# Kernel tuning notes

Hardware: AMD Instinct MI355X
Metric: run time of the kernel (lower is better)

## Reference

```python
import jax, jax.numpy as jnp
import numpy as np

N_NODES = 50000
N_EDGES = 800000
D = 128


def setup_inputs() -> dict:
    key = jax.random.key(0)
    ks = jax.random.split(key, 7)
    stdv = 1.0 / np.sqrt(D)
    inputs = jax.random.normal(ks[0], (N_NODES, D), dtype=jnp.float32)
    weight = jax.random.uniform(ks[1], (D, D), dtype=jnp.float32, minval=-stdv, maxval=stdv)
    bias = jax.random.uniform(ks[2], (D,), dtype=jnp.float32, minval=-stdv, maxval=stdv)
    alpha = jax.random.uniform(ks[3], (2, 1, 1), dtype=jnp.float32, minval=-3.0, maxval=3.0)
    adj_vals = jax.random.uniform(ks[4], (N_EDGES,), dtype=jnp.float32)
    adj_rows = jax.random.randint(ks[5], (N_EDGES,), 0, N_NODES, dtype=jnp.int32)
    adj_cols = jax.random.randint(ks[6], (N_EDGES,), 0, N_NODES, dtype=jnp.int32)
    return {"inputs": inputs, "weight": weight, "bias": bias, "alpha": alpha,
            "adj_vals": adj_vals, "adj_rows": adj_rows, "adj_cols": adj_cols}


def reference(inputs, weight, bias, alpha, adj_vals, adj_rows, adj_cols):
    n = inputs.shape[0]
    # support = inputs @ weight  (dense GEMM; spmm with dense lhs == matmul)
    support = inputs @ weight                                  # [N, D]
    # output = adj @ support  as COO SpMM: gather source rows, scale, scatter-add
    gathered = support[adj_cols] * adj_vals[:, None]           # [E, D]
    agg = jax.ops.segment_sum(gathered, adj_rows, num_segments=n)  # [N, D]
    # softmax-gated combine of [agg, inputs] (stack order: output first)
    gate = jax.nn.softmax(alpha, axis=0)                       # [2,1,1]
    out = agg * gate[0] + inputs * gate[1]                     # [N, D]
    return jax.nn.elu(out + bias)
```

## Files before the change

kernel.cpp:

```cpp
#include <hip/hip_runtime.h>

#define N_NODES 50000
#define N_EDGES 800000
#define D 128
#define CAP 128

typedef __attribute__((ext_vector_type(8))) short bf16x8;
typedef __attribute__((ext_vector_type(4))) float f32x4;
typedef __attribute__((ext_vector_type(4))) short short4v;

__device__ __forceinline__ short f2bf(float f) {
    unsigned u = __float_as_uint(f);
    unsigned r = u + 0x7FFFu + ((u >> 16) & 1u);
    return (short)(r >> 16);
}
__device__ __forceinline__ float bf2f(short s) {
    return __uint_as_float(((unsigned)(unsigned short)s) << 16);
}

#define SCAT_GROUPS 8
#define SCAT_BPG    392
__global__ __launch_bounds__(256) void gemm_scatter_kernel(
    const float* __restrict__ inp, const float* __restrict__ W,
    short* __restrict__ support,
    const int* __restrict__ rows, const int* __restrict__ cols,
    const float* __restrict__ vals,
    int* __restrict__ cnt, int2* __restrict__ buckets, int nGemmBlocks)
{
    if ((int)blockIdx.x >= nGemmBlocks) {
        const int sbid = (int)blockIdx.x - nGemmBlocks;
        const int g  = sbid & (SCAT_GROUPS - 1);
        const int gi = sbid >> 3;
        const int rowLo = g * (N_NODES / SCAT_GROUPS);
        const int rowHi = rowLo + (N_NODES / SCAT_GROUPS);
        for (int e = gi * 256 + threadIdx.x; e < N_EDGES; e += SCAT_BPG * 256) {
            int r = rows[e];
            if (r >= rowLo && r < rowHi) {
                int p = atomicAdd(&cnt[r], 1);
                if (p < CAP) {
                    int2 pk;
                    pk.x = cols[e];
                    pk.y = __float_as_int(vals[e]);
                    buckets[(size_t)r * CAP + p] = pk;
                }
            }
        }
        return;
    }

    __shared__ short Wt[128][136];
    const int tid = threadIdx.x;

    #pragma unroll
    for (int i = 0; i < 16; ++i) {
        int lin = i * 1024 + tid * 4;
        int k = lin >> 7, c = lin & 127;
        float4 w = *(const float4*)&W[lin];
        Wt[c + 0][k] = f2bf(w.x);
        Wt[c + 1][k] = f2bf(w.y);
        Wt[c + 2][k] = f2bf(w.z);
        Wt[c + 3][k] = f2bf(w.w);
    }
    __syncthreads();

    const int wid = tid >> 6, lane = tid & 63;
    const int lr = lane & 15;
    const int lg = lane >> 4;
    const int m0 = (int)blockIdx.x * 64 + wid * 16;

    int arow = m0 + lr;
    if (arow >= N_NODES) arow = 0;
    const float* aptr = &inp[(size_t)arow * D + lg * 8];

    f32x4 acc[8] = {};
    #pragma unroll
    for (int kc = 0; kc < 4; ++kc) {
        float4 a0 = *(const float4*)(aptr + kc * 32);
        float4 a1 = *(const float4*)(aptr + kc * 32 + 4);
        bf16x8 af;
        af[0] = f2bf(a0.x); af[1] = f2bf(a0.y); af[2] = f2bf(a0.z); af[3] = f2bf(a0.w);
        af[4] = f2bf(a1.x); af[5] = f2bf(a1.y); af[6] = f2bf(a1.z); af[7] = f2bf(a1.w);
        #pragma unroll
        for (int t = 0; t < 8; ++t) {
            const bf16x8 bf = *(const bf16x8*)&Wt[t * 16 + lr][kc * 32 + lg * 8];
            acc[t] = __builtin_amdgcn_mfma_f32_16x16x32_bf16(af, bf, acc[t], 0, 0, 0);
        }
    }
    #pragma unroll
    for (int t = 0; t < 8; ++t) {
        #pragma unroll
        for (int r = 0; r < 4; ++r) {
            int orow = m0 + lg * 4 + r;
            if (orow < N_NODES)
                support[(size_t)orow * D + t * 16 + lr] = f2bf(acc[t][r]);
        }
    }
}

__global__ __launch_bounds__(256) void agg_fused(
    const short* __restrict__ support, const int* __restrict__ cnt,
    const int2* __restrict__ buckets,
    const float* __restrict__ inp, const float* __restrict__ bias,
    const float* __restrict__ alpha, float* __restrict__ out)
{
    const int wv = (blockIdx.x * 256 + threadIdx.x) >> 6;
    const int lane = threadIdx.x & 63;
    if (wv >= N_NODES) return;
    const int half = lane >> 5;
    const int li = lane & 31;

    int n = cnt[wv];
    if (n > CAP) n = CAP;
    const int start = wv * CAP;
    const int end   = start + n;

    const float4 x = *(const float4*)&inp[(size_t)wv * D + li * 4];
    const float4 b4 = *(const float4*)&bias[li * 4];
    const float a0 = alpha[0], a1 = alpha[1];

    float4 acc = make_float4(0.f, 0.f, 0.f, 0.f);
    int e = start;
    for (; e + 8 <= end; e += 8) {
        int2 p0 = buckets[e + 0 + half];
        int2 p1 = buckets[e + 2 + half];
        int2 p2 = buckets[e + 4 + half];
        int2 p3 = buckets[e + 6 + half];
        short4v s0 = *(const short4v*)&support[(size_t)p0.x * D + li * 4];
        short4v s1 = *(const short4v*)&support[(size_t)p1.x * D + li * 4];
        short4v s2 = *(const short4v*)&support[(size_t)p2.x * D + li * 4];
        short4v s3 = *(const short4v*)&support[(size_t)p3.x * D + li * 4];
        float v0 = __int_as_float(p0.y), v1 = __int_as_float(p1.y);
        float v2 = __int_as_float(p2.y), v3 = __int_as_float(p3.y);
        acc.x += v0 * bf2f(s0[0]) + v1 * bf2f(s1[0]) + v2 * bf2f(s2[0]) + v3 * bf2f(s3[0]);
        acc.y += v0 * bf2f(s0[1]) + v1 * bf2f(s1[1]) + v2 * bf2f(s2[1]) + v3 * bf2f(s3[1]);
        acc.z += v0 * bf2f(s0[2]) + v1 * bf2f(s1[2]) + v2 * bf2f(s2[2]) + v3 * bf2f(s3[2]);
        acc.w += v0 * bf2f(s0[3]) + v1 * bf2f(s1[3]) + v2 * bf2f(s2[3]) + v3 * bf2f(s3[3]);
    }
    for (; e < end; e += 2) {
        int idx = e + half;
        int2 p = (idx < end) ? buckets[idx] : make_int2(0, 0);
        float v = __int_as_float(p.y);
        short4v s = *(const short4v*)&support[(size_t)p.x * D + li * 4];
        acc.x += v * bf2f(s[0]);
        acc.y += v * bf2f(s[1]);
        acc.z += v * bf2f(s[2]);
        acc.w += v * bf2f(s[3]);
    }

    acc.x += __shfl_xor(acc.x, 32);
    acc.y += __shfl_xor(acc.y, 32);
    acc.z += __shfl_xor(acc.z, 32);
    acc.w += __shfl_xor(acc.w, 32);

    const float m = fmaxf(a0, a1);
    const float e0 = __expf(a0 - m), e1 = __expf(a1 - m);
    const float inv = 1.f / (e0 + e1);
    const float g0 = e0 * inv, g1 = e1 * inv;

    float t0 = acc.x * g0 + x.x * g1 + b4.x;
    float t1 = acc.y * g0 + x.y * g1 + b4.y;
    float t2 = acc.z * g0 + x.z * g1 + b4.z;
    float t3 = acc.w * g0 + x.w * g1 + b4.w;
    float r0 = t0 > 0.f ? t0 : (__expf(t0) - 1.f);
    float r1 = t1 > 0.f ? t1 : (__expf(t1) - 1.f);
    float r2 = t2 > 0.f ? t2 : (__expf(t2) - 1.f);
    float r3 = t3 > 0.f ? t3 : (__expf(t3) - 1.f);

    float2 o = (half == 0) ? make_float2(r0, r1) : make_float2(r2, r3);
    *(float2*)&out[(size_t)wv * D + li * 4 + half * 2] = o;
}

extern "C" void kernel_launch(void* const* d_in, const int* in_sizes, int n_in,
                              void* d_out, int out_size, void* d_ws, size_t ws_size,
                              hipStream_t stream)
{
    const float* inp   = (const float*)d_in[0];
    const float* W     = (const float*)d_in[1];
    const float* bias  = (const float*)d_in[2];
    const float* alpha = (const float*)d_in[3];
    const float* vals  = (const float*)d_in[4];
    const int*   rows  = (const int*)d_in[5];
    const int*   cols  = (const int*)d_in[6];
    float* out = (float*)d_out;

    short* support = (short*)d_ws;
    int*   cnt     = (int*)(support + (size_t)N_NODES * D);
    int2*  buckets = (int2*)(cnt + N_NODES);

    const int nGemmBlocks = (N_NODES + 63) / 64;
    const int nScatBlocks = SCAT_GROUPS * SCAT_BPG;

    (void)hipMemsetAsync(cnt, 0, (size_t)N_NODES * sizeof(int), stream);

    gemm_scatter_kernel<<<nGemmBlocks + nScatBlocks, 256, 0, stream>>>(
        inp, W, support, rows, cols, vals, cnt, buckets, nGemmBlocks);
    agg_fused<<<(N_NODES * 64 + 255) / 256, 256, 0, stream>>>(
        support, cnt, buckets, inp, bias, alpha, out);
}
```

Measured before the change: 171.1 us.

## Precompute bf16 transposed weight in a prep kernel and flatten edge scatter

```diff
diff --git a/kernel.cpp b/kernel.cpp
--- a/kernel.cpp
+++ b/kernel.cpp
@@ -18,50 +18,78 @@
     return __uint_as_float(((unsigned)(unsigned short)s) << 16);
 }
 
+__global__ __launch_bounds__(256) void prep_zero(const float* __restrict__ W,
+                                                 short* __restrict__ Wt,
+                                                 int* __restrict__ cnt)
+{
+    const int b = blockIdx.x, t = threadIdx.x;
+    if (b < 8) {
+        __shared__ short Ls[128][17];
+        #pragma unroll
+        for (int i = 0; i < 8; ++i) {
+            int lin = i * 256 + t;
+            int kk = lin >> 7;
+            int c  = lin & 127;
+            Ls[c][kk] = f2bf(W[(b * 16 + kk) * 128 + c]);
+        }
+        __syncthreads();
+        #pragma unroll
+        for (int i = 0; i < 8; ++i) {
+            int lin = i * 256 + t;
+            int c  = lin >> 4;
+            int kk = lin & 15;
+            Wt[c * 128 + b * 16 + kk] = Ls[c][kk];
+        }
+    } else {
+        int idx = (b - 8) * 256 + t;
+        if (idx < N_NODES) cnt[idx] = 0;
+    }
+}
+
 #define SCAT_GROUPS 8
-#define SCAT_BPG    392
+#define SCAT_BPG    784
 __global__ __launch_bounds__(256) void gemm_scatter_kernel(
-    const float* __restrict__ inp, const float* __restrict__ W,
+    const float* __restrict__ inp, const short* __restrict__ Wt,
     short* __restrict__ support,
     const int* __restrict__ rows, const int* __restrict__ cols,
     const float* __restrict__ vals,
     int* __restrict__ cnt, int2* __restrict__ buckets, int nGemmBlocks)
 {
+    const int tid = threadIdx.x;
     if ((int)blockIdx.x >= nGemmBlocks) {
         const int sbid = (int)blockIdx.x - nGemmBlocks;
         const int g  = sbid & (SCAT_GROUPS - 1);
         const int gi = sbid >> 3;
         const int rowLo = g * (N_NODES / SCAT_GROUPS);
         const int rowHi = rowLo + (N_NODES / SCAT_GROUPS);
-        for (int e = gi * 256 + threadIdx.x; e < N_EDGES; e += SCAT_BPG * 256) {
-            int r = rows[e];
-            if (r >= rowLo && r < rowHi) {
-                int p = atomicAdd(&cnt[r], 1);
-                if (p < CAP) {
-                    int2 pk;
-                    pk.x = cols[e];
-                    pk.y = __float_as_int(vals[e]);
-                    buckets[(size_t)r * CAP + p] = pk;
-                }
-            }
+        const int base = gi * 1024;
+        int e0 = base + tid, e1 = e0 + 256, e2 = e0 + 512, e3 = e0 + 768;
+        int r0 = (e0 < N_EDGES) ? rows[e0] : -1;
+        int r1 = (e1 < N_EDGES) ? rows[e1] : -1;
+        int r2 = (e2 < N_EDGES) ? rows[e2] : -1;
+        int r3 = (e3 < N_EDGES) ? rows[e3] : -1;
+        if (r0 >= rowLo && r0 < rowHi) {
+            int p = atomicAdd(&cnt[r0], 1);
+            if (p < CAP) buckets[(size_t)r0 * CAP + p] =
+                make_int2(cols[e0], __float_as_int(vals[e0]));
+        }
+        if (r1 >= rowLo && r1 < rowHi) {
+            int p = atomicAdd(&cnt[r1], 1);
+            if (p < CAP) buckets[(size_t)r1 * CAP + p] =
+                make_int2(cols[e1], __float_as_int(vals[e1]));
+        }
+        if (r2 >= rowLo && r2 < rowHi) {
+            int p = atomicAdd(&cnt[r2], 1);
+            if (p < CAP) buckets[(size_t)r2 * CAP + p] =
+                make_int2(cols[e2], __float_as_int(vals[e2]));
+        }
+        if (r3 >= rowLo && r3 < rowHi) {
+            int p = atomicAdd(&cnt[r3], 1);
+            if (p < CAP) buckets[(size_t)r3 * CAP + p] =
+                make_int2(cols[e3], __float_as_int(vals[e3]));
         }
         return;
     }
-
-    __shared__ short Wt[128][136];
-    const int tid = threadIdx.x;
-
-    #pragma unroll
-    for (int i = 0; i < 16; ++i) {
-        int lin = i * 1024 + tid * 4;
-        int k = lin >> 7, c = lin & 127;
-        float4 w = *(const float4*)&W[lin];
-        Wt[c + 0][k] = f2bf(w.x);
-        Wt[c + 1][k] = f2bf(w.y);
-        Wt[c + 2][k] = f2bf(w.z);
-        Wt[c + 3][k] = f2bf(w.w);
-    }
-    __syncthreads();
 
     const int wid = tid >> 6, lane = tid & 63;
     const int lr = lane & 15;
@@ -72,18 +100,28 @@
     if (arow >= N_NODES) arow = 0;
     const float* aptr = &inp[(size_t)arow * D + lg * 8];
 
+    float4 a[8];
+    #pragma unroll
+    for (int kc = 0; kc < 4; ++kc) {
+        a[2 * kc + 0] = *(const float4*)(aptr + kc * 32);
+        a[2 * kc + 1] = *(const float4*)(aptr + kc * 32 + 4);
+    }
+    bf16x8 af[4];
+    #pragma unroll
+    for (int kc = 0; kc < 4; ++kc) {
+        af[kc][0] = f2bf(a[2*kc].x);   af[kc][1] = f2bf(a[2*kc].y);
+        af[kc][2] = f2bf(a[2*kc].z);   af[kc][3] = f2bf(a[2*kc].w);
+        af[kc][4] = f2bf(a[2*kc+1].x); af[kc][5] = f2bf(a[2*kc+1].y);
+        af[kc][6] = f2bf(a[2*kc+1].z); af[kc][7] = f2bf(a[2*kc+1].w);
+    }
+
     f32x4 acc[8] = {};
     #pragma unroll
     for (int kc = 0; kc < 4; ++kc) {
-        float4 a0 = *(const float4*)(aptr + kc * 32);
-        float4 a1 = *(const float4*)(aptr + kc * 32 + 4);
-        bf16x8 af;
-        af[0] = f2bf(a0.x); af[1] = f2bf(a0.y); af[2] = f2bf(a0.z); af[3] = f2bf(a0.w);
-        af[4] = f2bf(a1.x); af[5] = f2bf(a1.y); af[6] = f2bf(a1.z); af[7] = f2bf(a1.w);
         #pragma unroll
         for (int t = 0; t < 8; ++t) {
-            const bf16x8 bf = *(const bf16x8*)&Wt[t * 16 + lr][kc * 32 + lg * 8];
-            acc[t] = __builtin_amdgcn_mfma_f32_16x16x32_bf16(af, bf, acc[t], 0, 0, 0);
+            const bf16x8 bf = *(const bf16x8*)&Wt[(t * 16 + lr) * 128 + kc * 32 + lg * 8];
+            acc[t] = __builtin_amdgcn_mfma_f32_16x16x32_bf16(af[kc], bf, acc[t], 0, 0, 0);
         }
     }
     #pragma unroll
@@ -184,16 +222,16 @@
     float* out = (float*)d_out;
 
     short* support = (short*)d_ws;
-    int*   cnt     = (int*)(support + (size_t)N_NODES * D);
+    short* Wt      = support + (size_t)N_NODES * D;
+    int*   cnt     = (int*)(Wt + 128 * 128);
     int2*  buckets = (int2*)(cnt + N_NODES);
 
     const int nGemmBlocks = (N_NODES + 63) / 64;
     const int nScatBlocks = SCAT_GROUPS * SCAT_BPG;
 
-    (void)hipMemsetAsync(cnt, 0, (size_t)N_NODES * sizeof(int), stream);
-
+    prep_zero<<<8 + (N_NODES + 255) / 256, 256, 0, stream>>>(W, Wt, cnt);
     gemm_scatter_kernel<<<nGemmBlocks + nScatBlocks, 256, 0, stream>>>(
-        inp, W, support, rows, cols, vals, cnt, buckets, nGemmBlocks);
+        inp, Wt, support, rows, cols, vals, cnt, buckets, nGemmBlocks);
     agg_fused<<<(N_NODES * 64 + 255) / 256, 256, 0, stream>>>(
         support, cnt, buckets, inp, bias, alpha, out);
 }
```

New measurement: 175.6 us. 2.6% more time.
